# Optimization experiments

Hardware: AMD Instinct MI355X
Metric: run time of the kernel (lower is better)

Reference implementation:

```python
import jax, jax.numpy as jnp
import numpy as np
import math

B, S, DM = 2, 2048, 2048
NH, NKV, HD = 16, 4, 128
DFF = 8192
K_KEEP = DFF // 2  # sparsity_ratio = 0.5
EPS = 1e-6


def setup_inputs() -> dict:
    key = jax.random.key(0)
    ks = jax.random.split(key, 10)
    sc = 0.02
    return {
        "hidden_states": jax.random.normal(ks[0], (B, S, DM), dtype=jnp.float32),
        "wq": jax.random.normal(ks[1], (NH * HD, DM), dtype=jnp.float32) * sc,
        "wk": jax.random.normal(ks[2], (NKV * HD, DM), dtype=jnp.float32) * sc,
        "wv": jax.random.normal(ks[3], (NKV * HD, DM), dtype=jnp.float32) * sc,
        "wo": jax.random.normal(ks[4], (DM, NH * HD), dtype=jnp.float32) * sc,
        "ln1_w": jnp.ones((DM,), dtype=jnp.float32),
        "ln2_w": jnp.ones((DM,), dtype=jnp.float32),
        "w_gate": jax.random.normal(ks[5], (DFF, DM), dtype=jnp.float32) * sc,
        "w_up": jax.random.normal(ks[6], (DFF, DM), dtype=jnp.float32) * sc,
        "w_down": jax.random.normal(ks[7], (DM, DFF), dtype=jnp.float32) * sc,
    }


def _rmsnorm(x, w):
    var = jnp.mean(x * x, axis=-1, keepdims=True)
    return x * jax.lax.rsqrt(var + EPS) * w


def reference(hidden_states, wq, wk, wv, wo, ln1_w, ln2_w, w_gate, w_up, w_down):
    b, s, _ = hidden_states.shape
    # --- attention sub-block: RMSNorm -> GQA causal attention -> residual ---
    x = _rmsnorm(hidden_states, ln1_w)
    q = (x @ wq.T).reshape(b, s, NH, HD)
    k = (x @ wk.T).reshape(b, s, NKV, HD)
    v = (x @ wv.T).reshape(b, s, NKV, HD)
    # expand KV heads to match query heads (GQA)
    rep = NH // NKV
    k = jnp.repeat(k, rep, axis=2)
    v = jnp.repeat(v, rep, axis=2)
    scores = jnp.einsum('bqhd,bkhd->bhqk', q, k) / math.sqrt(HD)
    causal = jnp.tril(jnp.ones((s, s), dtype=bool))
    scores = jnp.where(causal, scores, jnp.finfo(scores.dtype).min)
    attn = jax.nn.softmax(scores, axis=-1)
    o = jnp.einsum('bhqk,bkhd->bqhd', attn, v).reshape(b, s, NH * HD)
    h = hidden_states + o @ wo.T
    # --- FFN sub-block: RMSNorm -> TopK-sparse SwiGLU -> residual ---
    y = _rmsnorm(h, ln2_w)
    gate = jax.nn.silu(y @ w_gate.T)  # [b, s, DFF]
    mag = jnp.abs(gate)
    thr = jax.lax.top_k(mag, K_KEEP)[0][..., -1:]  # kth-largest magnitude
    gate = jnp.where(mag >= thr, gate, 0.0)
    ff = (gate * (y @ w_up.T)) @ w_down.T
    return h + ff
```

## Files before the change

### kernel.cpp

```cpp
#include <hip/hip_runtime.h>
#include <stdint.h>

constexpr int SEQ    = 2048;
constexpr int DMODEL = 2048;
constexpr int NHEADS = 16;
constexpr int NKVH   = 4;
constexpr int HDIM   = 128;
constexpr int DFFN   = 8192;
constexpr int BATCH  = 2;
constexpr int MTOK   = BATCH * SEQ;
constexpr int KKEEP  = DFFN / 2;

typedef __bf16 bf16x8 __attribute__((ext_vector_type(8)));
typedef float  f32x4  __attribute__((ext_vector_type(4)));
typedef float  f32x16 __attribute__((ext_vector_type(16)));
typedef unsigned short u16;
typedef unsigned int   u32;

__device__ __forceinline__ u16 f2bu(float f) {
  u32 x = __builtin_bit_cast(u32, f);
  return (u16)((x + 0x7FFFu + ((x >> 16) & 1u)) >> 16);
}
__device__ __forceinline__ float b2f(u16 u) {
  u32 v = ((u32)u) << 16;
  return __builtin_bit_cast(float, v);
}
__device__ __forceinline__ void gl_lds16(const void* g, void* l) {
  __builtin_amdgcn_global_load_lds((const __attribute__((address_space(1))) u32*)g,
                                   (__attribute__((address_space(3))) u32*)l, 16, 0, 0);
}

__global__ __launch_bounds__(256) void cvt_kernel(const float* __restrict__ in,
                                                  u16* __restrict__ out, int n) {
  int i = (blockIdx.x * 256 + threadIdx.x) * 4;
  if (i >= n) return;
  float4 v = *(const float4*)(in + i);
  uint2 pk;
  pk.x = (u32)f2bu(v.x) | ((u32)f2bu(v.y) << 16);
  pk.y = (u32)f2bu(v.z) | ((u32)f2bu(v.w) << 16);
  *(uint2*)(out + i) = pk;
}

__global__ __launch_bounds__(256) void rmsnorm_kernel(const float* __restrict__ in,
                                                      const float* __restrict__ w,
                                                      u16* __restrict__ out) {
  const int tid = threadIdx.x;
  const size_t row = blockIdx.x;
  const float* x = in + row * DMODEL;
  float4 v0 = *(const float4*)(x + tid * 4);
  float4 v1 = *(const float4*)(x + 1024 + tid * 4);
  float s = v0.x*v0.x + v0.y*v0.y + v0.z*v0.z + v0.w*v0.w
          + v1.x*v1.x + v1.y*v1.y + v1.z*v1.z + v1.w*v1.w;
#pragma unroll
  for (int off = 1; off < 64; off <<= 1) s += __shfl_xor(s, off, 64);
  __shared__ float wsum[4];
  if ((tid & 63) == 0) wsum[tid >> 6] = s;
  __syncthreads();
  s = wsum[0] + wsum[1] + wsum[2] + wsum[3];
  const float rinv = rsqrtf(s * (1.0f / DMODEL) + 1e-6f);
  u16* o = out + row * DMODEL;
#pragma unroll
  for (int part = 0; part < 2; ++part) {
    int c = part * 1024 + tid * 4;
    float4 vv = (part == 0) ? v0 : v1;
    float4 wv = *(const float4*)(w + c);
    uint2 pk;
    pk.x = (u32)f2bu(vv.x * rinv * wv.x) | ((u32)f2bu(vv.y * rinv * wv.y) << 16);
    pk.y = (u32)f2bu(vv.z * rinv * wv.z) | ((u32)f2bu(vv.w * rinv * wv.w) << 16);
    *(uint2*)(o + c) = pk;
  }
}

template <int EPI>
__global__ __launch_bounds__(256, 2)
void gemm_bt(const u16* __restrict__ A, const u16* __restrict__ B,
             void* __restrict__ C, const float* res,
             int M, int N, int K) {
  __shared__ u16 As[128 * 64];
  __shared__ u16 Bs[128 * 64];
  const int tid = threadIdx.x;
  const int wave = tid >> 6, lane = tid & 63;
  const int nwg = gridDim.x * gridDim.y;
  const int lin = blockIdx.y * gridDim.x + blockIdx.x;
  const int swz = (lin & 7) * (nwg >> 3) + (lin >> 3);
  const int m0 = (swz / gridDim.x) * 128, n0 = (swz % gridDim.x) * 128;
  const int r_in = lane >> 3, chk = lane & 7;
  const int fk = lane >> 4, fc = lane & 15;
  const int wm = (wave >> 1) * 64, wn = (wave & 1) * 64;
  f32x4 acc[4][4] = {};

  for (int kt = 0; kt < K; kt += 64) {
    __syncthreads();
#pragma unroll
    for (int i = 0; i < 4; ++i) {
      int row = wave * 32 + i * 8 + r_in;
      int gc = chk ^ (row & 7);
      gl_lds16(A + (size_t)(m0 + row) * K + kt + gc * 8, As + (wave * 32 + i * 8) * 64);
    }
#pragma unroll
    for (int i = 0; i < 4; ++i) {
      int row = wave * 32 + i * 8 + r_in;
      int gc = chk ^ (row & 7);
      gl_lds16(B + (size_t)(n0 + row) * K + kt + gc * 8, Bs + (wave * 32 + i * 8) * 64);
    }
    __syncthreads();
#pragma unroll
    for (int kk = 0; kk < 2; ++kk) {
      bf16x8 a[4], b[4];
#pragma unroll
      for (int i = 0; i < 4; ++i) {
        int row = wm + i * 16 + fc;
        int c = (kk * 4 + fk) ^ (row & 7);
        a[i] = *(const bf16x8*)(As + row * 64 + c * 8);
      }
#pragma unroll
      for (int j = 0; j < 4; ++j) {
        int row = wn + j * 16 + fc;
        int c = (kk * 4 + fk) ^ (row & 7);
        b[j] = *(const bf16x8*)(Bs + row * 64 + c * 8);
      }
#pragma unroll
      for (int i = 0; i < 4; ++i)
#pragma unroll
        for (int j = 0; j < 4; ++j)
          acc[i][j] = __builtin_amdgcn_mfma_f32_16x16x32_bf16(a[i], b[j], acc[i][j], 0, 0, 0);
    }
  }

  const int rb = fk * 4;
#pragma unroll
  for (int i = 0; i < 4; ++i) {
#pragma unroll
    for (int j = 0; j < 4; ++j) {
      int row = m0 + wm + i * 16 + rb;
      int col = n0 + wn + j * 16 + fc;
      f32x4 v = acc[i][j];
      if constexpr (EPI == 0) {
        u16* o = (u16*)C;
#pragma unroll
        for (int r = 0; r < 4; ++r) o[(size_t)(row + r) * N + col] = f2bu(v[r]);
      } else if constexpr (EPI == 1) {
        u16* o = (u16*)C;
        int bb = row >> 11, s = row & (SEQ - 1);
        int kvh = col >> 7, d = col & (HDIM - 1);
        size_t base = (((size_t)bb * NKVH + kvh) * HDIM + d) * SEQ + s;
        uint2 pk;
        pk.x = (u32)f2bu(v[0]) | ((u32)f2bu(v[1]) << 16);
        pk.y = (u32)f2bu(v[2]) | ((u32)f2bu(v[3]) << 16);
        *(uint2*)(o + base) = pk;
      } else if constexpr (EPI == 2) {
        float* o = (float*)C;
#pragma unroll
        for (int r = 0; r < 4; ++r) {
          size_t idx = (size_t)(row + r) * N + col;
          float rv = res[idx];
          o[idx] = v[r] + rv;
        }
      } else {
        float* o = (float*)C;
#pragma unroll
        for (int r = 0; r < 4; ++r) {
          float g = v[r];
          o[(size_t)(row + r) * N + col] = g / (1.0f + __expf(-g));
        }
      }
    }
  }
}

__global__ __launch_bounds__(256, 2)
void attn_kernel(const u16* __restrict__ Q, const u16* __restrict__ Kb,
                 const u16* __restrict__ Vt, u16* __restrict__ O) {
  __shared__ u16 Ksh[2 * 32 * 128];
  __shared__ u16 Vsh[2 * 128 * 32];
  const int tid = threadIdx.x, wave = tid >> 6, lane = tid & 63;
  const int half = lane >> 5, l31 = lane & 31;
  const int d_lin = blockIdx.x + gridDim.x * (blockIdx.y + gridDim.y * blockIdx.z);
  const int lin = (d_lin & 7) * 64 + (d_lin >> 3);
  const int bx = lin & 15, h = (lin >> 4) & 15, b = lin >> 8;
  const int kvh = h >> 2;
  const int qw = bx * 128 + wave * 32;
  const float SC = 0.08838834764831845f;
  const int ntb = bx * 4 + 4;
  const int nmy = bx * 4 + wave;

  bf16x8 qf[8];
  {
    const u16* qp = Q + ((size_t)(b * SEQ + qw + l31)) * DMODEL + h * HDIM + half * 8;
#pragma unroll
    for (int s = 0; s < 8; ++s) qf[s] = *(const bf16x8*)(qp + s * 16);
  }
  f32x16 oacc[4] = {};
  float m_run = -1e30f, l_run = 0.0f;
  const size_t vbase = ((size_t)(b * NKVH + kvh)) * HDIM * SEQ;
  const u16* kbase = Kb + (size_t)b * SEQ * (NKVH * HDIM) + kvh * HDIM;

  auto stage = [&](int bi, int k0) {
    u16* Kd = Ksh + bi * 4096;
    u16* Vd = Vsh + bi * 4096;
#pragma unroll
    for (int ii = 0; ii < 2; ++ii) {
      int inst = wave * 2 + ii;
      {
        int row = inst * 4 + (lane >> 4);
        int c = (lane & 15) ^ (row & 15);
        gl_lds16(kbase + (size_t)(k0 + row) * (NKVH * HDIM) + c * 8, Kd + inst * 512);
      }
      {
        int row = inst * 16 + (lane >> 2);
        int c = (lane & 3) ^ ((row >> 1) & 3);
        gl_lds16(Vt + vbase + (size_t)row * SEQ + k0 + c * 8, Vd + inst * 512);
      }
    }
  };

  stage(0, 0);
  __syncthreads();

  for (int t = 0; t < ntb; ++t) {
    if (t + 1 < ntb) stage((t + 1) & 1, (t + 1) * 32);
    if (t <= nmy) {
      const u16* Kd = Ksh + (t & 1) * 4096;
      const u16* Vd = Vsh + (t & 1) * 4096;
      f32x16 st = {};
#pragma unroll
      for (int s = 0; s < 8; ++s) {
        int c = (half + 2 * s) ^ (l31 & 15);
        bf16x8 kf = *(const bf16x8*)(Kd + l31 * 128 + c * 8);
        st = __builtin_amdgcn_mfma_f32_32x32x16_bf16(kf, qf[s], st, 0, 0, 0);
      }
      const bool diag = (t * 32 == qw);
      float sv[16];
#pragma unroll
      for (int r = 0; r < 16; ++r) {
        float x = st[r] * SC;
        if (diag) {
          int kvl = (r & 3) + 8 * (r >> 2) + 4 * half;
          if (kvl > l31) x = -1e30f;
        }
        sv[r] = x;
      }
      float mx = sv[0];
#pragma unroll
      for (int r = 1; r < 16; ++r) mx = fmaxf(mx, sv[r]);
      mx = fmaxf(mx, __shfl_xor(mx, 32, 64));
      if (__any(mx > m_run + 4.0f)) {
        float mnew = fmaxf(m_run, mx);
        float alpha = __expf(m_run - mnew);
        m_run = mnew;
        l_run *= alpha;
#pragma unroll
        for (int r = 0; r < 16; ++r) {
          float ar = __shfl(alpha, (r & 3) + 8 * (r >> 2) + 4 * half, 64);
#pragma unroll
          for (int dt = 0; dt < 4; ++dt) oacc[dt][r] *= ar;
        }
      }
      float p[16];
      float rs = 0.0f;
#pragma unroll
      for (int r = 0; r < 16; ++r) { p[r] = __expf(sv[r] - m_run); rs += p[r]; }
      rs += __shfl_xor(rs, 32, 64);
      l_run += rs;
      u32 c01 = (u32)f2bu(p[0])  | ((u32)f2bu(p[1])  << 16);
      u32 c23 = (u32)f2bu(p[2])  | ((u32)f2bu(p[3])  << 16);
      u32 c45 = (u32)f2bu(p[4])  | ((u32)f2bu(p[5])  << 16);
      u32 c67 = (u32)f2bu(p[6])  | ((u32)f2bu(p[7])  << 16);
      u32 c89 = (u32)f2bu(p[8])  | ((u32)f2bu(p[9])  << 16);
      u32 cAB = (u32)f2bu(p[10]) | ((u32)f2bu(p[11]) << 16);
      u32 cCD = (u32)f2bu(p[12]) | ((u32)f2bu(p[13]) << 16);
      u32 cEF = (u32)f2bu(p[14]) | ((u32)f2bu(p[15]) << 16);
      u32 paw[2][4];
      {
        u32 sA = __shfl_xor(c01, 32, 64), sB = __shfl_xor(c23, 32, 64);
        u32 sC = __shfl_xor(c45, 32, 64), sD = __shfl_xor(c67, 32, 64);
        paw[0][0] = half ? sC : c01;  paw[0][1] = half ? sD : c23;
        paw[0][2] = half ? c45 : sA;  paw[0][3] = half ? c67 : sB;
      }
      {
        u32 sA = __shfl_xor(c89, 32, 64), sB = __shfl_xor(cAB, 32, 64);
        u32 sC = __shfl_xor(cCD, 32, 64), sD = __shfl_xor(cEF, 32, 64);
        paw[1][0] = half ? sC : c89;  paw[1][1] = half ? sD : cAB;
        paw[1][2] = half ? cCD : sA;  paw[1][3] = half ? cEF : sB;
      }
#pragma unroll
      for (int ks = 0; ks < 2; ++ks) {
        bf16x8 paf = __builtin_bit_cast(bf16x8, *(uint4*)&paw[ks][0]);
#pragma unroll
        for (int dt = 0; dt < 4; ++dt) {
          int row = dt * 32 + l31;
          int c = (half + 2 * ks) ^ ((row >> 1) & 3);
          bf16x8 vf = *(const bf16x8*)(Vd + row * 32 + c * 8);
          oacc[dt] = __builtin_amdgcn_mfma_f32_32x32x16_bf16(paf, vf, oacc[dt], 0, 0, 0);
        }
      }
    }
    __syncthreads();
  }

  float rinv = 1.0f / l_run;
  u16* ob = O + ((size_t)(b * SEQ + qw)) * DMODEL + h * HDIM + l31;
#pragma unroll
  for (int r = 0; r < 16; ++r) {
    int qr = (r & 3) + 8 * (r >> 2) + 4 * half;
    float ir = __shfl(rinv, qr, 64);
#pragma unroll
    for (int dt = 0; dt < 4; ++dt)
      ob[(size_t)qr * DMODEL + dt * 32] = f2bu(oacc[dt][r] * ir);
  }
}

__global__ __launch_bounds__(256)
void topk_kernel(const float* __restrict__ gate, u16* __restrict__ upact) {
  __shared__ u32 sabs[DFFN];
  __shared__ u32 hist[4][256];
  __shared__ u32 ss[257];
  __shared__ u32 sh_prefix, sh_rem;
  const int tid = threadIdx.x, wave = tid >> 6;
  const size_t row = blockIdx.x;
  const float* g = gate + row * DFFN;
  for (int it = 0; it < 4; ++it) {
    int e = it * 2048 + tid * 8;
    float4 a = *(const float4*)(g + e);
    float4 b = *(const float4*)(g + e + 4);
    sabs[e + 0] = __builtin_bit_cast(u32, a.x);
    sabs[e + 1] = __builtin_bit_cast(u32, a.y);
    sabs[e + 2] = __builtin_bit_cast(u32, a.z);
    sabs[e + 3] = __builtin_bit_cast(u32, a.w);
    sabs[e + 4] = __builtin_bit_cast(u32, b.x);
    sabs[e + 5] = __builtin_bit_cast(u32, b.y);
    sabs[e + 6] = __builtin_bit_cast(u32, b.z);
    sabs[e + 7] = __builtin_bit_cast(u32, b.w);
  }
  if (tid == 0) { sh_prefix = 0; sh_rem = KKEEP; }
  __syncthreads();
  for (int pass = 0; pass < 4; ++pass) {
    const int p = 24 - pass * 8;
    const u32 mask_hi = (pass == 0) ? 0u : (0xFFFFFFFFu << (p + 8));
    for (int i = tid; i < 1024; i += 256) ((u32*)hist)[i] = 0;
    __syncthreads();
    const u32 prefix = sh_prefix, rem = sh_rem;
    for (int it = 0; it < 4; ++it) {
      int e = it * 2048 + tid * 8;
#pragma unroll
      for (int j = 0; j < 8; ++j) {
        u32 mg = sabs[e + j] & 0x7FFFFFFFu;
        if ((mg & mask_hi) == (prefix & mask_hi))
          atomicAdd(&hist[wave][(mg >> p) & 0xFF], 1u);
      }
    }
    __syncthreads();
    ss[tid] = hist[0][tid] + hist[1][tid] + hist[2][tid] + hist[3][tid];
    if (tid == 0) ss[256] = 0;
    __syncthreads();
    for (int off = 1; off < 256; off <<= 1) {
      u32 v = (tid + off < 256) ? ss[tid + off] : 0u;
      __syncthreads();
      ss[tid] += v;
      __syncthreads();
    }
    if (ss[tid] >= rem && ss[tid + 1] < rem) {
      sh_prefix = prefix | ((u32)tid << p);
      sh_rem = rem - ss[tid + 1];
    }
    __syncthreads();
  }
  const u32 thr = sh_prefix;
  u16* ua = upact + row * DFFN;
  for (int it = 0; it < 4; ++it) {
    int e = it * 2048 + tid * 8;
    uint4 uv = *(const uint4*)(ua + e);
    const u16* up16 = (const u16*)&uv;
    u16 outp[8];
#pragma unroll
    for (int j = 0; j < 8; ++j) {
      u32 bits = sabs[e + j];
      u32 mg = bits & 0x7FFFFFFFu;
      float gg = __builtin_bit_cast(float, bits);
      float prod = (mg >= thr) ? gg * b2f(up16[j]) : 0.0f;
      outp[j] = f2bu(prod);
    }
    uint4 ov;
    ov.x = (u32)outp[0] | ((u32)outp[1] << 16);
    ov.y = (u32)outp[2] | ((u32)outp[3] << 16);
    ov.z = (u32)outp[4] | ((u32)outp[5] << 16);
    ov.w = (u32)outp[6] | ((u32)outp[7] << 16);
    *(uint4*)(ua + e) = ov;
  }
}

extern "C" void kernel_launch(void* const* d_in, const int* in_sizes, int n_in,
                              void* d_out, int out_size, void* d_ws, size_t ws_size,
                              hipStream_t stream) {
  const float* hidden = (const float*)d_in[0];
  const float* wq = (const float*)d_in[1];
  const float* wk = (const float*)d_in[2];
  const float* wv = (const float*)d_in[3];
  const float* wo = (const float*)d_in[4];
  const float* ln1 = (const float*)d_in[5];
  const float* ln2 = (const float*)d_in[6];
  const float* wg = (const float*)d_in[7];
  const float* wu = (const float*)d_in[8];
  const float* wd = (const float*)d_in[9];
  float* out = (float*)d_out;
  (void)in_sizes; (void)n_in; (void)out_size;

  size_t off = 0;
  auto alloc = [&](size_t n) { char* r = (char*)d_ws + off; off += (n + 255) & ~(size_t)255; return r; };
  u16* wq_b = (u16*)alloc((size_t)DMODEL * DMODEL * 2);
  u16* wk_b = (u16*)alloc((size_t)NKVH * HDIM * DMODEL * 2);
  u16* wv_b = (u16*)alloc((size_t)NKVH * HDIM * DMODEL * 2);
  u16* wo_b = (u16*)alloc((size_t)DMODEL * DMODEL * 2);
  u16* wg_b = (u16*)alloc((size_t)DFFN * DMODEL * 2);
  u16* tok  = (u16*)alloc((size_t)MTOK * DMODEL * 2);
  u16* upb  = (u16*)alloc((size_t)MTOK * DFFN * 2);
  char* S   = alloc((size_t)(MTOK / 2) * DFFN * 4);
  u16* qb   = (u16*)S;
  u16* kb   = (u16*)(S + (size_t)MTOK * DMODEL * 2);
  u16* vtb  = (u16*)(S + (size_t)MTOK * DMODEL * 2 + (size_t)MTOK * NKVH * HDIM * 2);
  u16* wu_b = (u16*)(S + (size_t)MTOK * DMODEL * 2 + 2 * (size_t)MTOK * NKVH * HDIM * 2);
  float* gateh = (float*)S;
  u16* wd_b = (u16*)S;
  const size_t needed = off;
  if (ws_size < needed) return;

  auto cvt = [&](const float* src, u16* dst, size_t n) {
    cvt_kernel<<<dim3((unsigned)(n / 1024)), 256, 0, stream>>>(src, dst, (int)n);
  };
  cvt(wq, wq_b, (size_t)DMODEL * DMODEL);
  cvt(wk, wk_b, (size_t)NKVH * HDIM * DMODEL);
  cvt(wv, wv_b, (size_t)NKVH * HDIM * DMODEL);
  cvt(wo, wo_b, (size_t)DMODEL * DMODEL);
  cvt(wg, wg_b, (size_t)DFFN * DMODEL);
  cvt(wu, wu_b, (size_t)DFFN * DMODEL);

  rmsnorm_kernel<<<MTOK, 256, 0, stream>>>(hidden, ln1, tok);

  gemm_bt<0><<<dim3(DMODEL / 128, MTOK / 128), 256, 0, stream>>>(
      tok, wq_b, qb, nullptr, MTOK, DMODEL, DMODEL);
  gemm_bt<0><<<dim3(NKVH * HDIM / 128, MTOK / 128), 256, 0, stream>>>(
      tok, wk_b, kb, nullptr, MTOK, NKVH * HDIM, DMODEL);
  gemm_bt<1><<<dim3(NKVH * HDIM / 128, MTOK / 128), 256, 0, stream>>>(
      tok, wv_b, vtb, nullptr, MTOK, NKVH * HDIM, DMODEL);

  attn_kernel<<<dim3(SEQ / 128, NHEADS, BATCH), 256, 0, stream>>>(qb, kb, vtb, tok);

  gemm_bt<2><<<dim3(DMODEL / 128, MTOK / 128), 256, 0, stream>>>(
      tok, wo_b, out, hidden, MTOK, DMODEL, DMODEL);

  rmsnorm_kernel<<<MTOK, 256, 0, stream>>>(out, ln2, tok);

  gemm_bt<0><<<dim3(DFFN / 128, MTOK / 128), 256, 0, stream>>>(
      tok, wu_b, upb, nullptr, MTOK, DFFN, DMODEL);

  for (int half = 0; half < 2; ++half) {
    const u16* yh = tok + (size_t)half * (MTOK / 2) * DMODEL;
    u16* uph = upb + (size_t)half * (MTOK / 2) * DFFN;
    gemm_bt<3><<<dim3(DFFN / 128, (MTOK / 2) / 128), 256, 0, stream>>>(
        yh, wg_b, gateh, nullptr, MTOK / 2, DFFN, DMODEL);
    topk_kernel<<<MTOK / 2, 256, 0, stream>>>(gateh, uph);
  }

  cvt(wd, wd_b, (size_t)DMODEL * DFFN);

  gemm_bt<2><<<dim3(DMODEL / 128, MTOK / 128), 256, 0, stream>>>(
      upb, wd_b, out, out, MTOK, DMODEL, DFFN);
}
```

Measured before the change: 1.086 ms.

## Pipeline GEMM K-loop with four-stage LDS ring buffer and async prefetch

Replaces the single-buffered 64-wide K tile in the bf16 GEMM with a 4-deep ring of 32-wide K tiles. Global-to-LDS loads for three tiles ahead are issued before compute, and partial vmcnt waits plus one barrier per step replace the two full syncthreads. The LDS layout and swizzle change to a paired-row scheme to suit the narrower tile. The aim is to hide global memory latency behind MFMA work, at the cost of more barrier steps and a tighter reliance on wait counts for correctness.

```diff
diff --git a/kernel.cpp b/kernel.cpp
--- a/kernel.cpp
+++ b/kernel.cpp
@@ -76,55 +76,62 @@
 void gemm_bt(const u16* __restrict__ A, const u16* __restrict__ B,
              void* __restrict__ C, const float* res,
              int M, int N, int K) {
-  __shared__ u16 As[128 * 64];
-  __shared__ u16 Bs[128 * 64];
+  __shared__ u16 As[4][128 * 32];
+  __shared__ u16 Bs[4][128 * 32];
   const int tid = threadIdx.x;
   const int wave = tid >> 6, lane = tid & 63;
   const int nwg = gridDim.x * gridDim.y;
   const int lin = blockIdx.y * gridDim.x + blockIdx.x;
   const int swz = (lin & 7) * (nwg >> 3) + (lin >> 3);
   const int m0 = (swz / gridDim.x) * 128, n0 = (swz % gridDim.x) * 128;
-  const int r_in = lane >> 3, chk = lane & 7;
   const int fk = lane >> 4, fc = lane & 15;
   const int wm = (wave >> 1) * 64, wn = (wave & 1) * 64;
+  const int nt = K >> 5;
   f32x4 acc[4][4] = {};
 
-  for (int kt = 0; kt < K; kt += 64) {
-    __syncthreads();
-#pragma unroll
-    for (int i = 0; i < 4; ++i) {
-      int row = wave * 32 + i * 8 + r_in;
-      int gc = chk ^ (row & 7);
-      gl_lds16(A + (size_t)(m0 + row) * K + kt + gc * 8, As + (wave * 32 + i * 8) * 64);
-    }
-#pragma unroll
-    for (int i = 0; i < 4; ++i) {
-      int row = wave * 32 + i * 8 + r_in;
-      int gc = chk ^ (row & 7);
-      gl_lds16(B + (size_t)(n0 + row) * K + kt + gc * 8, Bs + (wave * 32 + i * 8) * 64);
-    }
-    __syncthreads();
-#pragma unroll
-    for (int kk = 0; kk < 2; ++kk) {
-      bf16x8 a[4], b[4];
-#pragma unroll
-      for (int i = 0; i < 4; ++i) {
-        int row = wm + i * 16 + fc;
-        int c = (kk * 4 + fk) ^ (row & 7);
-        a[i] = *(const bf16x8*)(As + row * 64 + c * 8);
-      }
-#pragma unroll
-      for (int j = 0; j < 4; ++j) {
-        int row = wn + j * 16 + fc;
-        int c = (kk * 4 + fk) ^ (row & 7);
-        b[j] = *(const bf16x8*)(Bs + row * 64 + c * 8);
-      }
-#pragma unroll
-      for (int i = 0; i < 4; ++i)
-#pragma unroll
-        for (int j = 0; j < 4; ++j)
-          acc[i][j] = __builtin_amdgcn_mfma_f32_16x16x32_bf16(a[i], b[j], acc[i][j], 0, 0, 0);
-    }
+  const int sU0 = wave * 128 + lane;
+  auto stage = [&](int buf, int t) {
+    const int kt = t * 32;
+#pragma unroll
+    for (int ii = 0; ii < 2; ++ii) {
+      const int i = wave * 2 + ii;
+      const int U = sU0 + ii * 64;
+      const int rp = U >> 3, w = U & 7;
+      const int c = (w >> 1) ^ (rp & 3);
+      const int row = (rp << 1) | (w & 1);
+      gl_lds16(A + (size_t)(m0 + row) * K + kt + c * 8, &As[buf][i * 512]);
+      gl_lds16(B + (size_t)(n0 + row) * K + kt + c * 8, &Bs[buf][i * 512]);
+    }
+  };
+
+  stage(0, 0); stage(1, 1); stage(2, 2);
+  asm volatile("s_waitcnt vmcnt(8)" ::: "memory");
+  __builtin_amdgcn_s_barrier();
+
+  for (int t = 0; t < nt; ++t) {
+    if (t + 3 < nt) stage((t + 3) & 3, t + 3);
+    const u16* Ab = As[t & 3];
+    const u16* Bb = Bs[t & 3];
+    bf16x8 a[4], b[4];
+#pragma unroll
+    for (int m = 0; m < 4; ++m) {
+      int row = wm + m * 16 + fc;
+      int U = ((row >> 1) << 3) + ((fk ^ ((row >> 1) & 3)) << 1) + (row & 1);
+      a[m] = *(const bf16x8*)(Ab + U * 8);
+    }
+#pragma unroll
+    for (int j = 0; j < 4; ++j) {
+      int row = wn + j * 16 + fc;
+      int U = ((row >> 1) << 3) + ((fk ^ ((row >> 1) & 3)) << 1) + (row & 1);
+      b[j] = *(const bf16x8*)(Bb + U * 8);
+    }
+#pragma unroll
+    for (int m = 0; m < 4; ++m)
+#pragma unroll
+      for (int j = 0; j < 4; ++j)
+        acc[m][j] = __builtin_amdgcn_mfma_f32_16x16x32_bf16(a[m], b[j], acc[m][j], 0, 0, 0);
+    asm volatile("s_waitcnt vmcnt(8)" ::: "memory");
+    __builtin_amdgcn_s_barrier();
   }
 
   const int rb = fk * 4;
```

Measured after the change: 1.197 ms. 10.2% more time.
